# Performance work log

Measured on AMD Instinct MI355X. Metric: run time of the kernel, lower is better.

## Reference

```python
import jax, jax.numpy as jnp
import numpy as np

E, D, H, K = 8, 768, 3072, 2   # num_experts, embed_size, expert_size, top-k
TAU = 1.0
BN, PN = 32, 196

def l2norm(v):
    # F.normalize(p=2, dim=-1), eps=1e-12
    return v / jnp.maximum(jnp.linalg.norm(v, axis=-1, keepdims=True), 1e-12)

def setup_inputs() -> dict:
    key = jax.random.key(0)
    ks = jax.random.split(key, 8)
    s = 0.02  # weight init scale for stability
    return {
        "x": jax.random.normal(ks[0], (BN, PN, D), dtype=jnp.float32),
        "Wlinear": jax.random.normal(ks[1], (D, D), dtype=jnp.float32) * s,
        "learnedE": jax.random.normal(ks[2], (E, D), dtype=jnp.float32),
        "bias": jnp.zeros((BN * PN, E), dtype=jnp.float32),
        "W1": jax.random.normal(ks[3], (E, D, H), dtype=jnp.float32) * s,
        "b1": jnp.zeros((E, H), dtype=jnp.float32),
        "W2": jax.random.normal(ks[4], (E, H, D), dtype=jnp.float32) * s,
        "b2": jnp.zeros((E, D), dtype=jnp.float32),
        "sW1": jax.random.normal(ks[5], (D, H), dtype=jnp.float32) * s,
        "sb1": jnp.zeros((H,), dtype=jnp.float32),
        "sW2": jax.random.normal(ks[6], (H, D), dtype=jnp.float32) * s,
        "sb2": jnp.zeros((D,), dtype=jnp.float32),
    }

def reference(x, Wlinear, learnedE, bias, W1, b1, W2, b2, sW1, sb1, sW2, sb2):
    bn, pn, d = x.shape
    patches = x.reshape(bn * pn, d)                      # [T, D]
    proj = l2norm(patches @ Wlinear.T)                   # router projection
    routed = proj @ l2norm(learnedE).T                   # [T, E] cosine scores
    probs = jax.nn.softmax((routed + bias) / TAU, axis=1)  # eval path (no noise)
    k_probs, k_idx = jax.lax.top_k(probs, K)             # [T, K]
    # combine weights: scatter top-k probs into dense [T, E] gate matrix
    T = probs.shape[0]
    gates = jnp.zeros_like(probs).at[jnp.arange(T)[:, None], k_idx].add(k_probs)
    # expert MLPs computed densely for all experts, masked by gates
    h = jax.nn.gelu(jnp.einsum('td,edh->teh', patches, W1) + b1[None], approximate=False)
    eo = jnp.einsum('teh,ehd->ted', h, W2) + b2[None]    # [T, E, D]
    moe = jnp.einsum('ted,te->td', eo, gates)            # weighted combine
    # shared expert (expert_list[-1]) applied to every token; dropout is identity in eval
    shared = jax.nn.gelu(patches @ sW1 + sb1, approximate=False) @ sW2 + sb2
    return (moe + shared).reshape(bn, pn, d)
```

## Files before the change

kernel.cpp:

```cpp
#include <hip/hip_runtime.h>
#include <hip/hip_bf16.h>

typedef __hip_bfloat16 bf16;
typedef __attribute__((ext_vector_type(8))) short short8;
typedef __attribute__((ext_vector_type(4))) float f32x4;

#define T_TOK 6272
#define D_DIM 768
#define H_DIM 3072
#define NEXP 8
#define MAXTILES 160
#define BKR 64

#define S_BARRIER() __builtin_amdgcn_s_barrier()
#define WAIT_VM0() asm volatile("s_waitcnt vmcnt(0)" ::: "memory")

__device__ __forceinline__ void async16(void* lds, const void* g) {
  __builtin_amdgcn_global_load_lds(
      (const __attribute__((address_space(1))) void*)g,
      (__attribute__((address_space(3))) void*)lds, 16, 0, 0);
}

__device__ __forceinline__ float gelu_f(float x) {
  float z = x * 0.70710678118654752f;
  float az = fabsf(z);
  float t = 1.f / (1.f + 0.3275911f * az);
  float poly = ((((1.061405429f * t - 1.453152027f) * t + 1.421413741f) * t -
                 0.284496736f) * t + 0.254829592f) * t;
  float e = __expf(-az * az);
  float er = 1.f - poly * e;
  er = copysignf(er, z);
  return 0.5f * x * (1.f + er);
}


__global__ void cast_hilo(const float* __restrict__ in, bf16* __restrict__ hi,
                          bf16* __restrict__ lo, int n) {
  int i = blockIdx.x * blockDim.x + threadIdx.x;
  int stride = gridDim.x * blockDim.x;
  for (; i < n; i += stride) {
    float x = in[i];
    bf16 h = __float2bfloat16(x);
    hi[i] = h;
    lo[i] = __float2bfloat16(x - __bfloat162float(h));
  }
}

__global__ void transpose_cast(const float* __restrict__ in, bf16* __restrict__ out,
                               int R, int C) {
  __shared__ float tile[32][33];
  int b = blockIdx.z;
  const float* ib = in + (size_t)b * R * C;
  bf16* ob = out + (size_t)b * R * C;
  int r0 = blockIdx.x * 32, c0 = blockIdx.y * 32;
  int tx = threadIdx.x & 31, ty = threadIdx.x >> 5;
  for (int i = 0; i < 32; i += 8)
    tile[ty + i][tx] = ib[(size_t)(r0 + ty + i) * C + c0 + tx];
  __syncthreads();
  for (int i = 0; i < 32; i += 8)
    ob[(size_t)(c0 + ty + i) * R + r0 + tx] = __float2bfloat16(tile[tx][ty + i]);
}

__global__ void norm_learnedE(const float* __restrict__ lE, float* __restrict__ eHat) {
  int wave = threadIdx.x >> 6, lane = threadIdx.x & 63;
  for (int e = wave; e < NEXP; e += 4) {
    float v[12];
    float ss = 0.f;
    for (int j = 0; j < 12; j++) {
      v[j] = lE[e * D_DIM + lane + 64 * j];
      ss += v[j] * v[j];
    }
    for (int o = 32; o; o >>= 1) ss += __shfl_xor(ss, o);
    float rn = 1.f / fmaxf(sqrtf(ss), 1e-12f);
    for (int j = 0; j < 12; j++) eHat[e * D_DIM + lane + 64 * j] = v[j] * rn;
  }
}


__global__ __launch_bounds__(256, 2) void gemm_router(
    const bf16* __restrict__ pHi, const bf16* __restrict__ pLo,
    const bf16* __restrict__ wHi, const bf16* __restrict__ wLo,
    float* __restrict__ y) {
  __shared__ __align__(16) bf16 As[2][128 * BKR];
  __shared__ __align__(16) bf16 Bs[2][128 * BKR];
  int tid = threadIdx.x, wave = tid >> 6, lane = tid & 63;
  int wr = wave >> 1, wc = wave & 1;
  int rowbase = blockIdx.x * 128, colbase = blockIdx.y * 128;
  int rslot = (lane & 7) ^ (lane >> 3);

  size_t aoff[4], boff[4];
#pragma unroll
  for (int c = 0; c < 4; c++) {
    int row = 32 * wave + 8 * c + (lane >> 3);
    aoff[c] = (size_t)(rowbase + row) * D_DIM + rslot * 8;
    boff[c] = (size_t)(colbase + row) * D_DIM + rslot * 8;
  }

  auto stage = [&](int buf, int ks) {
    int term = ks / 12;
    const bf16* A = (term == 1) ? pLo : pHi;
    const bf16* B = (term == 2) ? wLo : wHi;
    int kk = (ks - term * 12) * BKR;
#pragma unroll
    for (int c = 0; c < 4; c++) {
      async16(&As[buf][(32 * wave + 8 * c) * BKR], A + aoff[c] + kk);
      async16(&Bs[buf][(32 * wave + 8 * c) * BKR], B + boff[c] + kk);
    }
  };

  f32x4 acc[4][4];
#pragma unroll
  for (int m = 0; m < 4; m++)
#pragma unroll
    for (int n = 0; n < 4; n++) acc[m][n] = 0.f;

  stage(0, 0);
  __syncthreads();
  int cur = 0;
  int q = lane >> 4, fr = lane & 15;
  for (int ks = 0; ks < 36; ks++) {
    if (ks < 35) stage(cur ^ 1, ks + 1);
    const bf16* Ac = As[cur];
    const bf16* Bc = Bs[cur];
#pragma unroll
    for (int kh = 0; kh < 2; kh++) {
      short8 af[4], bfr[4];
#pragma unroll
      for (int m = 0; m < 4; m++) {
        int row = wr * 64 + m * 16 + fr;
        int ls = ((kh << 2) + q) ^ (row & 7);
        af[m] = *(const short8*)&Ac[row * BKR + ls * 8];
      }
#pragma unroll
      for (int n = 0; n < 4; n++) {
        int row = wc * 64 + n * 16 + fr;
        int ls = ((kh << 2) + q) ^ (row & 7);
        bfr[n] = *(const short8*)&Bc[row * BKR + ls * 8];
      }
#pragma unroll
      for (int m = 0; m < 4; m++)
#pragma unroll
        for (int n = 0; n < 4; n++)
          acc[m][n] = __builtin_amdgcn_mfma_f32_16x16x32_bf16(af[m], bfr[n], acc[m][n], 0, 0, 0);
    }
    __syncthreads();
    cur ^= 1;
  }
  for (int m = 0; m < 4; m++)
    for (int n = 0; n < 4; n++)
      for (int j = 0; j < 4; j++) {
        int r = rowbase + wr * 64 + m * 16 + (lane >> 4) * 4 + j;
        int c = colbase + wc * 64 + n * 16 + (lane & 15);
        y[(size_t)r * D_DIM + c] = acc[m][n][j];
      }
}


__global__ void router_epi(const float* __restrict__ y, const float* __restrict__ eHat,
                           const float* __restrict__ bias, int* __restrict__ gidx,
                           float* __restrict__ gval, int* __restrict__ counts) {
  int wave = threadIdx.x >> 6, lane = threadIdx.x & 63;
  int t = blockIdx.x * 4 + wave;
  float v[12];
  float ss = 0.f;
  for (int j = 0; j < 12; j++) {
    v[j] = y[(size_t)t * D_DIM + lane + 64 * j];
    ss += v[j] * v[j];
  }
  for (int o = 32; o; o >>= 1) ss += __shfl_xor(ss, o);
  float d[NEXP];
  for (int e = 0; e < NEXP; e++) {
    float s = 0.f;
    for (int j = 0; j < 12; j++) s += v[j] * eHat[e * D_DIM + lane + 64 * j];
    for (int o = 32; o; o >>= 1) s += __shfl_xor(s, o);
    d[e] = s;
  }
  if (lane == 0) {
    float rn = 1.f / fmaxf(sqrtf(ss), 1e-12f);
    float sc[NEXP], mx = -1e30f;
    for (int e = 0; e < NEXP; e++) {
      sc[e] = d[e] * rn + bias[t * NEXP + e];
      mx = fmaxf(mx, sc[e]);
    }
    float p[NEXP], sum = 0.f;
    for (int e = 0; e < NEXP; e++) {
      p[e] = expf(sc[e] - mx);
      sum += p[e];
    }
    float inv = 1.f / sum;
    int i1 = 0;
    for (int e = 1; e < NEXP; e++)
      if (sc[e] > sc[i1]) i1 = e;
    int i2 = -1;
    for (int e = 0; e < NEXP; e++) {
      if (e == i1) continue;
      if (i2 < 0 || sc[e] > sc[i2]) i2 = e;
    }
    gidx[t * 2] = i1;
    gidx[t * 2 + 1] = i2;
    gval[t * 2] = p[i1] * inv;
    gval[t * 2 + 1] = p[i2] * inv;
    atomicAdd(&counts[i1], 1);
    atomicAdd(&counts[i2], 1);
  }
}


__global__ void scan_build(const int* __restrict__ counts, int* __restrict__ segstart,
                           int* __restrict__ cursors, int* __restrict__ tiles,
                           int* __restrict__ numtiles) {
  if (threadIdx.x == 0) {
    int off = 0;
    for (int e = 0; e < NEXP; e++) {
      segstart[e] = off;
      cursors[e] = off;
      off += counts[e];
    }
    segstart[NEXP] = off;
    segstart[NEXP + 1] = off + T_TOK;
    int nt = 0;
    for (int e = 0; e < NEXP + 1; e++) {
      int cnt = (e < NEXP) ? counts[e] : T_TOK;
      int ntl = (cnt + 127) >> 7;
      for (int l = 0; l < ntl; l++) {
        tiles[nt * 2] = e;
        tiles[nt * 2 + 1] = l;
        nt++;
      }
    }
    *numtiles = nt;
  }
}

__global__ void fill_assign(const int* __restrict__ gidx, int* __restrict__ cursors,
                            int* __restrict__ rowtok, int* __restrict__ slot_of) {
  int t = blockIdx.x * 256 + threadIdx.x;
  if (t >= T_TOK) return;
  for (int k = 0; k < 2; k++) {
    int e = gidx[t * 2 + k];
    int pos = atomicAdd(&cursors[e], 1);
    rowtok[pos] = t;
    slot_of[t * 2 + k] = pos;
  }
  rowtok[2 * T_TOK + t] = t;
}



__global__ __launch_bounds__(256, 4) void gemm_ffn1(
    const bf16* __restrict__ pHi, const bf16* __restrict__ W1T,
    const bf16* __restrict__ sW1T, const float* __restrict__ b1,
    const float* __restrict__ sb1, const int* __restrict__ segstart,
    const int* __restrict__ tiles, const int* __restrict__ numtiles,
    const int* __restrict__ rowtok, bf16* __restrict__ hbuf) {
  int gx = blockIdx.x;
  if (gx >= *numtiles) return;
  int seg = tiles[gx * 2], lt = tiles[gx * 2 + 1];
  int s0 = segstart[seg] + lt * 128;
  int send = segstart[seg + 1];
  const bf16* Bw = (seg < NEXP) ? W1T + (size_t)seg * H_DIM * D_DIM : sW1T;
  const float* bb = (seg < NEXP) ? b1 + seg * H_DIM : sb1;

  __shared__ __align__(16) bf16 As[2][128 * 32];
  __shared__ __align__(16) bf16 Bs[2][128 * 32];
  int tid = threadIdx.x, wave = tid >> 6, lane = tid & 63;
  int wr = wave >> 1, wc = wave & 1;
  int colbase = blockIdx.y * 128;
  int q = lane >> 4, fr = lane & 15;
  int g8 = (((lane & 3) ^ ((lane >> 3) & 3))) * 8;
  int ls8 = (q ^ ((fr >> 1) & 3)) * 8;

  const bf16* aptr[2];
  const bf16* bptr[2];
#pragma unroll
  for (int p = 0; p < 2; p++) {
    int r = wave * 32 + p * 16 + (lane >> 2);
    int s = s0 + r;
    if (s > send - 1) s = send - 1;
    aptr[p] = pHi + (size_t)rowtok[s] * D_DIM + g8;
    bptr[p] = Bw + (size_t)(colbase + r) * D_DIM + g8;
  }

  auto stage = [&](int buf, int ks) {
    int kk = ks * 32;
#pragma unroll
    for (int p = 0; p < 2; p++) {
      async16(&As[buf][(wave * 32 + p * 16) * 32], aptr[p] + kk);
      async16(&Bs[buf][(wave * 32 + p * 16) * 32], bptr[p] + kk);
    }
  };

  f32x4 acc[4][4];
#pragma unroll
  for (int m = 0; m < 4; m++)
#pragma unroll
    for (int n = 0; n < 4; n++) acc[m][n] = 0.f;

  stage(0, 0);
  WAIT_VM0();
  S_BARRIER();

#define NT1 24
  for (int ks = 0; ks < NT1; ks++) {
    if (ks + 1 < NT1) stage((ks + 1) & 1, ks + 1);
    const bf16* Ac = As[ks & 1];
    const bf16* Bc = Bs[ks & 1];
    short8 af[4], bfr[4];
#pragma unroll
    for (int m = 0; m < 4; m++)
      af[m] = *(const short8*)&Ac[(wr * 64 + m * 16 + fr) * 32 + ls8];
#pragma unroll
    for (int n = 0; n < 4; n++)
      bfr[n] = *(const short8*)&Bc[(wc * 64 + n * 16 + fr) * 32 + ls8];
    __builtin_amdgcn_s_setprio(1);
#pragma unroll
    for (int m = 0; m < 4; m++)
#pragma unroll
      for (int n = 0; n < 4; n++)
        acc[m][n] = __builtin_amdgcn_mfma_f32_16x16x32_bf16(af[m], bfr[n], acc[m][n], 0, 0, 0);
    __builtin_amdgcn_s_setprio(0);
    WAIT_VM0();
    S_BARRIER();
  }
#pragma unroll
  for (int n = 0; n < 4; n++) {
    int c = colbase + wc * 64 + n * 16 + fr;
    float bv = bb[c];
#pragma unroll
    for (int m = 0; m < 4; m++)
#pragma unroll
      for (int j = 0; j < 4; j++) {
        int s = s0 + wr * 64 + m * 16 + q * 4 + j;
        if (s < send) {
          float xv = acc[m][n][j] + bv;
          hbuf[(size_t)s * H_DIM + c] = __float2bfloat16(gelu_f(xv));
        }
      }
  }
}


__global__ __launch_bounds__(256, 4) void gemm_ffn2(
    const bf16* __restrict__ hbuf, const bf16* __restrict__ W2T,
    const bf16* __restrict__ sW2T, const float* __restrict__ b2,
    const float* __restrict__ sb2, const int* __restrict__ segstart,
    const int* __restrict__ tiles, const int* __restrict__ numtiles,
    float* __restrict__ moebuf) {
  int gx = blockIdx.x;
  if (gx >= *numtiles) return;
  int seg = tiles[gx * 2], lt = tiles[gx * 2 + 1];
  int s0 = segstart[seg] + lt * 128;
  int send = segstart[seg + 1];
  const bf16* Bw = (seg < NEXP) ? W2T + (size_t)seg * H_DIM * D_DIM : sW2T;
  const float* bb = (seg < NEXP) ? b2 + seg * D_DIM : sb2;

  __shared__ __align__(16) bf16 As[2][128 * 32];
  __shared__ __align__(16) bf16 Bs[2][128 * 32];
  int tid = threadIdx.x, wave = tid >> 6, lane = tid & 63;
  int wr = wave >> 1, wc = wave & 1;
  int colbase = blockIdx.y * 128;
  int q = lane >> 4, fr = lane & 15;
  int g8 = (((lane & 3) ^ ((lane >> 3) & 3))) * 8;
  int ls8 = (q ^ ((fr >> 1) & 3)) * 8;

  const bf16* aptr[2];
  const bf16* bptr[2];
#pragma unroll
  for (int p = 0; p < 2; p++) {
    int r = wave * 32 + p * 16 + (lane >> 2);
    int s = s0 + r;
    if (s > send - 1) s = send - 1;
    aptr[p] = hbuf + (size_t)s * H_DIM + g8;
    bptr[p] = Bw + (size_t)(colbase + r) * H_DIM + g8;
  }

  auto stage = [&](int buf, int ks) {
    int kk = ks * 32;
#pragma unroll
    for (int p = 0; p < 2; p++) {
      async16(&As[buf][(wave * 32 + p * 16) * 32], aptr[p] + kk);
      async16(&Bs[buf][(wave * 32 + p * 16) * 32], bptr[p] + kk);
    }
  };

  f32x4 acc[4][4];
#pragma unroll
  for (int m = 0; m < 4; m++)
#pragma unroll
    for (int n = 0; n < 4; n++) acc[m][n] = 0.f;

  stage(0, 0);
  WAIT_VM0();
  S_BARRIER();

#define NT2 96
  for (int ks = 0; ks < NT2; ks++) {
    if (ks + 1 < NT2) stage((ks + 1) & 1, ks + 1);
    const bf16* Ac = As[ks & 1];
    const bf16* Bc = Bs[ks & 1];
    short8 af[4], bfr[4];
#pragma unroll
    for (int m = 0; m < 4; m++)
      af[m] = *(const short8*)&Ac[(wr * 64 + m * 16 + fr) * 32 + ls8];
#pragma unroll
    for (int n = 0; n < 4; n++)
      bfr[n] = *(const short8*)&Bc[(wc * 64 + n * 16 + fr) * 32 + ls8];
    __builtin_amdgcn_s_setprio(1);
#pragma unroll
    for (int m = 0; m < 4; m++)
#pragma unroll
      for (int n = 0; n < 4; n++)
        acc[m][n] = __builtin_amdgcn_mfma_f32_16x16x32_bf16(af[m], bfr[n], acc[m][n], 0, 0, 0);
    __builtin_amdgcn_s_setprio(0);
    WAIT_VM0();
    S_BARRIER();
  }
#pragma unroll
  for (int n = 0; n < 4; n++) {
    int c = colbase + wc * 64 + n * 16 + fr;
    float bv = bb[c];
#pragma unroll
    for (int m = 0; m < 4; m++)
#pragma unroll
      for (int j = 0; j < 4; j++) {
        int s = s0 + wr * 64 + m * 16 + q * 4 + j;
        if (s < send) moebuf[(size_t)s * D_DIM + c] = acc[m][n][j] + bv;
      }
  }
}


__global__ void combine_out(const float* __restrict__ moebuf, const float* __restrict__ gval,
                            const int* __restrict__ slot_of, float* __restrict__ out) {
  int i = blockIdx.x * 256 + threadIdx.x;
  const int total = T_TOK * (D_DIM / 4);
  if (i >= total) return;
  int t = i / (D_DIM / 4), c = i % (D_DIM / 4);
  float g0 = gval[2 * t], g1 = gval[2 * t + 1];
  int sA = slot_of[2 * t], sB = slot_of[2 * t + 1];
  const f32x4* pa = (const f32x4*)(moebuf + (size_t)sA * D_DIM) + c;
  const f32x4* pb = (const f32x4*)(moebuf + (size_t)sB * D_DIM) + c;
  const f32x4* ps = (const f32x4*)(moebuf + (size_t)(2 * T_TOK + t) * D_DIM) + c;
  f32x4 r = g0 * (*pa) + g1 * (*pb) + *ps;
  ((f32x4*)out)[i] = r;
}


extern "C" void kernel_launch(void* const* d_in, const int* in_sizes, int n_in,
                              void* d_out, int out_size, void* d_ws, size_t ws_size,
                              hipStream_t stream) {
  const float* x = (const float*)d_in[0];
  const float* Wlinear = (const float*)d_in[1];
  const float* learnedE = (const float*)d_in[2];
  const float* bias = (const float*)d_in[3];
  const float* W1 = (const float*)d_in[4];
  const float* b1 = (const float*)d_in[5];
  const float* W2 = (const float*)d_in[6];
  const float* b2 = (const float*)d_in[7];
  const float* sW1 = (const float*)d_in[8];
  const float* sb1 = (const float*)d_in[9];
  const float* sW2 = (const float*)d_in[10];
  const float* sb2 = (const float*)d_in[11];
  float* out = (float*)d_out;

  char* ws = (char*)d_ws;
  size_t off = 0;
  auto alloc = [&](size_t bytes) {
    char* p = ws + off;
    off += (bytes + 255) & ~(size_t)255;
    return p;
  };
  float* eHat = (float*)alloc(8 * 768 * 4);
  bf16* pHi = (bf16*)alloc((size_t)T_TOK * D_DIM * 2);
  bf16* pLo = (bf16*)alloc((size_t)T_TOK * D_DIM * 2);
  bf16* wHi = (bf16*)alloc((size_t)D_DIM * D_DIM * 2);
  bf16* wLo = (bf16*)alloc((size_t)D_DIM * D_DIM * 2);
  bf16* W1T = (bf16*)alloc((size_t)NEXP * D_DIM * H_DIM * 2);
  bf16* W2T = (bf16*)alloc((size_t)NEXP * D_DIM * H_DIM * 2);
  bf16* sW1T = (bf16*)alloc((size_t)D_DIM * H_DIM * 2);
  bf16* sW2T = (bf16*)alloc((size_t)D_DIM * H_DIM * 2);
  float* y = (float*)alloc((size_t)T_TOK * D_DIM * 4);
  bf16* hbuf = (bf16*)alloc((size_t)3 * T_TOK * H_DIM * 2);
  float* moebuf = (float*)alloc((size_t)3 * T_TOK * D_DIM * 4);
  int* gidx = (int*)alloc(T_TOK * 2 * 4);
  float* gval = (float*)alloc(T_TOK * 2 * 4);
  int* rowtok = (int*)alloc(3 * T_TOK * 4);
  int* slot_of = (int*)alloc(T_TOK * 2 * 4);
  int* counts = (int*)alloc(8 * 4);
  int* segstart = (int*)alloc(10 * 4);
  int* cursors = (int*)alloc(8 * 4);
  int* numtiles = (int*)alloc(4);
  int* tiles = (int*)alloc(MAXTILES * 2 * 4);
  (void)ws_size; (void)in_sizes; (void)n_in; (void)out_size;

  hipMemsetAsync(counts, 0, 8 * 4, stream);
  norm_learnedE<<<1, 256, 0, stream>>>(learnedE, eHat);
  cast_hilo<<<2048, 256, 0, stream>>>(x, pHi, pLo, T_TOK * D_DIM);
  cast_hilo<<<1024, 256, 0, stream>>>(Wlinear, wHi, wLo, D_DIM * D_DIM);
  transpose_cast<<<dim3(D_DIM / 32, H_DIM / 32, NEXP), 256, 0, stream>>>(W1, W1T, D_DIM, H_DIM);
  transpose_cast<<<dim3(H_DIM / 32, D_DIM / 32, NEXP), 256, 0, stream>>>(W2, W2T, H_DIM, D_DIM);
  transpose_cast<<<dim3(D_DIM / 32, H_DIM / 32, 1), 256, 0, stream>>>(sW1, sW1T, D_DIM, H_DIM);
  transpose_cast<<<dim3(H_DIM / 32, D_DIM / 32, 1), 256, 0, stream>>>(sW2, sW2T, H_DIM, D_DIM);

  gemm_router<<<dim3(T_TOK / 128, D_DIM / 128), 256, 0, stream>>>(pHi, pLo, wHi, wLo, y);
  router_epi<<<T_TOK / 4, 256, 0, stream>>>(y, eHat, bias, gidx, gval, counts);
  scan_build<<<1, 64, 0, stream>>>(counts, segstart, cursors, tiles, numtiles);
  fill_assign<<<(T_TOK + 255) / 256, 256, 0, stream>>>(gidx, cursors, rowtok, slot_of);

  gemm_ffn1<<<dim3(MAXTILES, H_DIM / 128), 256, 0, stream>>>(
      pHi, W1T, sW1T, b1, sb1, segstart, tiles, numtiles, rowtok, hbuf);
  gemm_ffn2<<<dim3(MAXTILES, D_DIM / 128), 256, 0, stream>>>(
      hbuf, W2T, sW2T, b2, sb2, segstart, tiles, numtiles, moebuf);

  combine_out<<<(T_TOK * (D_DIM / 4) + 255) / 256, 256, 0, stream>>>(moebuf, gval, slot_of, out);
}
```

Before: 719.1 us.

## Enlarge grouped FFN GEMM tiles to 256x256 with deeper async LDS pipeline

Both expert FFN GEMMs move from 128x128 tiles with 256 threads to 256x256 tiles with 512 threads. Each tile row is now 256 tokens, so the tile list and launch grid shrink to match. The double-buffered K loop becomes a 4-buffer pipeline: A and B loads are issued as separate half-stages and waited on with partial vmcnt counts, and each wave's 8x4 accumulator block is computed in two halves. The goal is more operand reuse per global load and more latency hiding. In exchange it uses about 128KB of LDS per block and more accumulator registers, and launches far fewer blocks (the FFN2 grid in particular may not fill the GPU).

```diff
diff --git a/kernel.cpp b/kernel.cpp
--- a/kernel.cpp
+++ b/kernel.cpp
@@ -9,10 +9,12 @@
 #define D_DIM 768
 #define H_DIM 3072
 #define NEXP 8
-#define MAXTILES 160
+#define MAXT 96
 #define BKR 64
 
 #define S_BARRIER() __builtin_amdgcn_s_barrier()
+#define WAIT_VM6() asm volatile("s_waitcnt vmcnt(6)" ::: "memory")
+#define WAIT_VM4() asm volatile("s_waitcnt vmcnt(4)" ::: "memory")
 #define WAIT_VM0() asm volatile("s_waitcnt vmcnt(0)" ::: "memory")
 
 __device__ __forceinline__ void async16(void* lds, const void* g) {
@@ -221,7 +223,7 @@
     int nt = 0;
     for (int e = 0; e < NEXP + 1; e++) {
       int cnt = (e < NEXP) ? counts[e] : T_TOK;
-      int ntl = (cnt + 127) >> 7;
+      int ntl = (cnt + 255) >> 8;
       for (int l = 0; l < ntl; l++) {
         tiles[nt * 2] = e;
         tiles[nt * 2 + 1] = l;
@@ -247,7 +249,7 @@
 
 
 
-__global__ __launch_bounds__(256, 4) void gemm_ffn1(
+__global__ __launch_bounds__(512, 2) void gemm_ffn1(
     const bf16* __restrict__ pHi, const bf16* __restrict__ W1T,
     const bf16* __restrict__ sW1T, const float* __restrict__ b1,
     const float* __restrict__ sb1, const int* __restrict__ segstart,
@@ -256,62 +258,67 @@
   int gx = blockIdx.x;
   if (gx >= *numtiles) return;
   int seg = tiles[gx * 2], lt = tiles[gx * 2 + 1];
-  int s0 = segstart[seg] + lt * 128;
+  int s0 = segstart[seg] + lt * 256;
   int send = segstart[seg + 1];
   const bf16* Bw = (seg < NEXP) ? W1T + (size_t)seg * H_DIM * D_DIM : sW1T;
   const float* bb = (seg < NEXP) ? b1 + seg * H_DIM : sb1;
 
-  __shared__ __align__(16) bf16 As[2][128 * 32];
-  __shared__ __align__(16) bf16 Bs[2][128 * 32];
+  __shared__ __align__(16) bf16 As[4][256 * 32];
+  __shared__ __align__(16) bf16 Bs[4][256 * 32];
   int tid = threadIdx.x, wave = tid >> 6, lane = tid & 63;
-  int wr = wave >> 1, wc = wave & 1;
-  int colbase = blockIdx.y * 128;
+  int wr = wave >> 2, wc = wave & 3;
+  int colbase = blockIdx.y * 256;
   int q = lane >> 4, fr = lane & 15;
-  int g8 = (((lane & 3) ^ ((lane >> 3) & 3))) * 8;
+  int g8 = ((tid & 3) ^ ((tid >> 3) & 3)) * 8;
+  int row0 = tid >> 2;
+  int slot8 = (tid & 3) * 8;
   int ls8 = (q ^ ((fr >> 1) & 3)) * 8;
 
-  const bf16* aptr[2];
-  const bf16* bptr[2];
-#pragma unroll
-  for (int p = 0; p < 2; p++) {
-    int r = wave * 32 + p * 16 + (lane >> 2);
-    int s = s0 + r;
-    if (s > send - 1) s = send - 1;
-    aptr[p] = pHi + (size_t)rowtok[s] * D_DIM + g8;
-    bptr[p] = Bw + (size_t)(colbase + r) * D_DIM + g8;
-  }
-
-  auto stage = [&](int buf, int ks) {
-    int kk = ks * 32;
-#pragma unroll
-    for (int p = 0; p < 2; p++) {
-      async16(&As[buf][(wave * 32 + p * 16) * 32], aptr[p] + kk);
-      async16(&Bs[buf][(wave * 32 + p * 16) * 32], bptr[p] + kk);
+  int sA0 = s0 + row0; if (sA0 > send - 1) sA0 = send - 1;
+  int sA1 = s0 + row0 + 128; if (sA1 > send - 1) sA1 = send - 1;
+  const bf16* aptr0 = pHi + (size_t)rowtok[sA0] * D_DIM + g8;
+  const bf16* aptr1 = pHi + (size_t)rowtok[sA1] * D_DIM + g8;
+  const bf16* bptr0 = Bw + (size_t)(colbase + row0) * D_DIM + g8;
+  const bf16* bptr1 = Bw + (size_t)(colbase + row0 + 128) * D_DIM + g8;
+
+  auto stage = [&](int s) {
+    int ts = s >> 1;
+    int kk = ts * 32;
+    int buf = ts & 3;
+    if ((s & 1) == 0) {
+      async16(&As[buf][row0 * 32 + slot8], aptr0 + kk);
+      async16(&As[buf][(row0 + 128) * 32 + slot8], aptr1 + kk);
+    } else {
+      async16(&Bs[buf][row0 * 32 + slot8], bptr0 + kk);
+      async16(&Bs[buf][(row0 + 128) * 32 + slot8], bptr1 + kk);
     }
   };
 
-  f32x4 acc[4][4];
-#pragma unroll
-  for (int m = 0; m < 4; m++)
+  f32x4 acc[8][4];
+#pragma unroll
+  for (int m = 0; m < 8; m++)
 #pragma unroll
     for (int n = 0; n < 4; n++) acc[m][n] = 0.f;
 
-  stage(0, 0);
   WAIT_VM0();
-  S_BARRIER();
+  stage(0); stage(1); stage(2); stage(3); stage(4);
 
 #define NT1 24
-  for (int ks = 0; ks < NT1; ks++) {
-    if (ks + 1 < NT1) stage((ks + 1) & 1, ks + 1);
-    const bf16* Ac = As[ks & 1];
-    const bf16* Bc = Bs[ks & 1];
-    short8 af[4], bfr[4];
-#pragma unroll
-    for (int m = 0; m < 4; m++)
-      af[m] = *(const short8*)&Ac[(wr * 64 + m * 16 + fr) * 32 + ls8];
+  for (int t = 0; t < NT1; t++) {
+    if (t + 2 < NT1) { WAIT_VM6(); }
+    else if (t + 1 < NT1) { WAIT_VM4(); }
+    else { WAIT_VM0(); }
+    S_BARRIER();
+    const bf16* Ac = As[t & 3];
+    const bf16* Bc = Bs[t & 3];
+    short8 bfr[4], af[4];
 #pragma unroll
     for (int n = 0; n < 4; n++)
       bfr[n] = *(const short8*)&Bc[(wc * 64 + n * 16 + fr) * 32 + ls8];
+#pragma unroll
+    for (int m = 0; m < 4; m++)
+      af[m] = *(const short8*)&Ac[(wr * 128 + m * 16 + fr) * 32 + ls8];
+    if (2 * t + 5 < 2 * NT1) stage(2 * t + 5);
     __builtin_amdgcn_s_setprio(1);
 #pragma unroll
     for (int m = 0; m < 4; m++)
@@ -319,7 +326,19 @@
       for (int n = 0; n < 4; n++)
         acc[m][n] = __builtin_amdgcn_mfma_f32_16x16x32_bf16(af[m], bfr[n], acc[m][n], 0, 0, 0);
     __builtin_amdgcn_s_setprio(0);
-    WAIT_VM0();
+    S_BARRIER();
+#pragma unroll
+    for (int m = 0; m < 4; m++)
+      af[m] = *(const short8*)&Ac[(wr * 128 + (m + 4) * 16 + fr) * 32 + ls8];
+    if (2 * t + 6 < 2 * NT1) stage(2 * t + 6);
+    S_BARRIER();
+    __builtin_amdgcn_s_setprio(1);
+#pragma unroll
+    for (int m = 0; m < 4; m++)
+#pragma unroll
+      for (int n = 0; n < 4; n++)
+        acc[m + 4][n] = __builtin_amdgcn_mfma_f32_16x16x32_bf16(af[m], bfr[n], acc[m + 4][n], 0, 0, 0);
+    __builtin_amdgcn_s_setprio(0);
     S_BARRIER();
   }
 #pragma unroll
@@ -327,10 +346,10 @@
     int c = colbase + wc * 64 + n * 16 + fr;
     float bv = bb[c];
 #pragma unroll
-    for (int m = 0; m < 4; m++)
+    for (int m = 0; m < 8; m++)
 #pragma unroll
       for (int j = 0; j < 4; j++) {
-        int s = s0 + wr * 64 + m * 16 + q * 4 + j;
+        int s = s0 + wr * 128 + m * 16 + q * 4 + j;
         if (s < send) {
           float xv = acc[m][n][j] + bv;
           hbuf[(size_t)s * H_DIM + c] = __float2bfloat16(gelu_f(xv));
@@ -340,7 +359,7 @@
 }
 
 
-__global__ __launch_bounds__(256, 4) void gemm_ffn2(
+__global__ __launch_bounds__(512, 2) void gemm_ffn2(
     const bf16* __restrict__ hbuf, const bf16* __restrict__ W2T,
     const bf16* __restrict__ sW2T, const float* __restrict__ b2,
     const float* __restrict__ sb2, const int* __restrict__ segstart,
@@ -349,62 +368,67 @@
   int gx = blockIdx.x;
   if (gx >= *numtiles) return;
   int seg = tiles[gx * 2], lt = tiles[gx * 2 + 1];
-  int s0 = segstart[seg] + lt * 128;
+  int s0 = segstart[seg] + lt * 256;
   int send = segstart[seg + 1];
   const bf16* Bw = (seg < NEXP) ? W2T + (size_t)seg * H_DIM * D_DIM : sW2T;
   const float* bb = (seg < NEXP) ? b2 + seg * D_DIM : sb2;
 
-  __shared__ __align__(16) bf16 As[2][128 * 32];
-  __shared__ __align__(16) bf16 Bs[2][128 * 32];
+  __shared__ __align__(16) bf16 As[4][256 * 32];
+  __shared__ __align__(16) bf16 Bs[4][256 * 32];
   int tid = threadIdx.x, wave = tid >> 6, lane = tid & 63;
-  int wr = wave >> 1, wc = wave & 1;
-  int colbase = blockIdx.y * 128;
+  int wr = wave >> 2, wc = wave & 3;
+  int colbase = blockIdx.y * 256;
   int q = lane >> 4, fr = lane & 15;
-  int g8 = (((lane & 3) ^ ((lane >> 3) & 3))) * 8;
+  int g8 = ((tid & 3) ^ ((tid >> 3) & 3)) * 8;
+  int row0 = tid >> 2;
+  int slot8 = (tid & 3) * 8;
   int ls8 = (q ^ ((fr >> 1) & 3)) * 8;
 
-  const bf16* aptr[2];
-  const bf16* bptr[2];
-#pragma unroll
-  for (int p = 0; p < 2; p++) {
-    int r = wave * 32 + p * 16 + (lane >> 2);
-    int s = s0 + r;
-    if (s > send - 1) s = send - 1;
-    aptr[p] = hbuf + (size_t)s * H_DIM + g8;
-    bptr[p] = Bw + (size_t)(colbase + r) * H_DIM + g8;
-  }
-
-  auto stage = [&](int buf, int ks) {
-    int kk = ks * 32;
-#pragma unroll
-    for (int p = 0; p < 2; p++) {
-      async16(&As[buf][(wave * 32 + p * 16) * 32], aptr[p] + kk);
-      async16(&Bs[buf][(wave * 32 + p * 16) * 32], bptr[p] + kk);
+  int sA0 = s0 + row0; if (sA0 > send - 1) sA0 = send - 1;
+  int sA1 = s0 + row0 + 128; if (sA1 > send - 1) sA1 = send - 1;
+  const bf16* aptr0 = hbuf + (size_t)sA0 * H_DIM + g8;
+  const bf16* aptr1 = hbuf + (size_t)sA1 * H_DIM + g8;
+  const bf16* bptr0 = Bw + (size_t)(colbase + row0) * H_DIM + g8;
+  const bf16* bptr1 = Bw + (size_t)(colbase + row0 + 128) * H_DIM + g8;
+
+  auto stage = [&](int s) {
+    int ts = s >> 1;
+    int kk = ts * 32;
+    int buf = ts & 3;
+    if ((s & 1) == 0) {
+      async16(&As[buf][row0 * 32 + slot8], aptr0 + kk);
+      async16(&As[buf][(row0 + 128) * 32 + slot8], aptr1 + kk);
+    } else {
+      async16(&Bs[buf][row0 * 32 + slot8], bptr0 + kk);
+      async16(&Bs[buf][(row0 + 128) * 32 + slot8], bptr1 + kk);
     }
   };
 
-  f32x4 acc[4][4];
-#pragma unroll
-  for (int m = 0; m < 4; m++)
+  f32x4 acc[8][4];
+#pragma unroll
+  for (int m = 0; m < 8; m++)
 #pragma unroll
     for (int n = 0; n < 4; n++) acc[m][n] = 0.f;
 
-  stage(0, 0);
   WAIT_VM0();
-  S_BARRIER();
+  stage(0); stage(1); stage(2); stage(3); stage(4);
 
 #define NT2 96
-  for (int ks = 0; ks < NT2; ks++) {
-    if (ks + 1 < NT2) stage((ks + 1) & 1, ks + 1);
-    const bf16* Ac = As[ks & 1];
-    const bf16* Bc = Bs[ks & 1];
-    short8 af[4], bfr[4];
-#pragma unroll
-    for (int m = 0; m < 4; m++)
-      af[m] = *(const short8*)&Ac[(wr * 64 + m * 16 + fr) * 32 + ls8];
+  for (int t = 0; t < NT2; t++) {
+    if (t + 2 < NT2) { WAIT_VM6(); }
+    else if (t + 1 < NT2) { WAIT_VM4(); }
+    else { WAIT_VM0(); }
+    S_BARRIER();
+    const bf16* Ac = As[t & 3];
+    const bf16* Bc = Bs[t & 3];
+    short8 bfr[4], af[4];
 #pragma unroll
     for (int n = 0; n < 4; n++)
       bfr[n] = *(const short8*)&Bc[(wc * 64 + n * 16 + fr) * 32 + ls8];
+#pragma unroll
+    for (int m = 0; m < 4; m++)
+      af[m] = *(const short8*)&Ac[(wr * 128 + m * 16 + fr) * 32 + ls8];
+    if (2 * t + 5 < 2 * NT2) stage(2 * t + 5);
     __builtin_amdgcn_s_setprio(1);
 #pragma unroll
     for (int m = 0; m < 4; m++)
@@ -412,7 +436,19 @@
       for (int n = 0; n < 4; n++)
         acc[m][n] = __builtin_amdgcn_mfma_f32_16x16x32_bf16(af[m], bfr[n], acc[m][n], 0, 0, 0);
     __builtin_amdgcn_s_setprio(0);
-    WAIT_VM0();
+    S_BARRIER();
+#pragma unroll
+    for (int m = 0; m < 4; m++)
+      af[m] = *(const short8*)&Ac[(wr * 128 + (m + 4) * 16 + fr) * 32 + ls8];
+    if (2 * t + 6 < 2 * NT2) stage(2 * t + 6);
+    S_BARRIER();
+    __builtin_amdgcn_s_setprio(1);
+#pragma unroll
+    for (int m = 0; m < 4; m++)
+#pragma unroll
+      for (int n = 0; n < 4; n++)
+        acc[m + 4][n] = __builtin_amdgcn_mfma_f32_16x16x32_bf16(af[m], bfr[n], acc[m + 4][n], 0, 0, 0);
+    __builtin_amdgcn_s_setprio(0);
     S_BARRIER();
   }
 #pragma unroll
@@ -420,10 +456,10 @@
     int c = colbase + wc * 64 + n * 16 + fr;
     float bv = bb[c];
 #pragma unroll
-    for (int m = 0; m < 4; m++)
+    for (int m = 0; m < 8; m++)
 #pragma unroll
       for (int j = 0; j < 4; j++) {
-        int s = s0 + wr * 64 + m * 16 + q * 4 + j;
+        int s = s0 + wr * 128 + m * 16 + q * 4 + j;
         if (s < send) moebuf[(size_t)s * D_DIM + c] = acc[m][n][j] + bv;
       }
   }
@@ -490,7 +526,7 @@
   int* segstart = (int*)alloc(10 * 4);
   int* cursors = (int*)alloc(8 * 4);
   int* numtiles = (int*)alloc(4);
-  int* tiles = (int*)alloc(MAXTILES * 2 * 4);
+  int* tiles = (int*)alloc(MAXT * 2 * 4);
   (void)ws_size; (void)in_sizes; (void)n_in; (void)out_size;
 
   hipMemsetAsync(counts, 0, 8 * 4, stream);
@@ -507,9 +543,9 @@
   scan_build<<<1, 64, 0, stream>>>(counts, segstart, cursors, tiles, numtiles);
   fill_assign<<<(T_TOK + 255) / 256, 256, 0, stream>>>(gidx, cursors, rowtok, slot_of);
 
-  gemm_ffn1<<<dim3(MAXTILES, H_DIM / 128), 256, 0, stream>>>(
+  gemm_ffn1<<<dim3(MAXT, H_DIM / 256), 512, 0, stream>>>(
       pHi, W1T, sW1T, b1, sb1, segstart, tiles, numtiles, rowtok, hbuf);
-  gemm_ffn2<<<dim3(MAXTILES, D_DIM / 128), 256, 0, stream>>>(
+  gemm_ffn2<<<dim3(MAXT, D_DIM / 256), 512, 0, stream>>>(
       hbuf, W2T, sW2T, b2, sb2, segstart, tiles, numtiles, moebuf);
 
   combine_out<<<(T_TOK * (D_DIM / 4) + 255) / 256, 256, 0, stream>>>(moebuf, gval, slot_of, out);
```

Measured after the change: 804.7 us. +11.9%, slower.

## Remap GEMM block indices for XCD-aware grouped tile scheduling

Applied to the files above, without the earlier changes.

Adds an XCD-aware remapping of linear block IDs so consecutive work items land on the same XCD. Within each XCD, tiles are swizzled into groups of row tiles sharing column tiles. This applies to the router GEMM and both expert FFN GEMMs, which now launch with flattened or reshaped grids. The aim is better L2 reuse of A and B tiles on MI355X's multi-XCD layout, at the cost of some index arithmetic and a dependence on the round-robin block-to-XCD dispatch assumption.

```diff
diff --git a/kernel.cpp b/kernel.cpp
--- a/kernel.cpp
+++ b/kernel.cpp
@@ -31,6 +31,13 @@
   float er = 1.f - poly * e;
   er = copysignf(er, z);
   return 0.5f * x * (1.f + er);
+}
+
+__device__ __forceinline__ int xcd_work(int orig, int nwr) {
+  if (orig >= nwr) return -1;
+  int xcd = orig & 7, pos = orig >> 3;
+  int q = nwr >> 3, r = nwr & 7;
+  return (xcd < r ? xcd * (q + 1) : r * (q + 1) + (xcd - r) * q) + pos;
 }
 
 
@@ -81,11 +88,19 @@
     const bf16* __restrict__ pHi, const bf16* __restrict__ pLo,
     const bf16* __restrict__ wHi, const bf16* __restrict__ wLo,
     float* __restrict__ y) {
+  int work = xcd_work(blockIdx.x, 294);
+  int tileG = work / 48;
+  int rem = work - tileG * 48;
+  int base = tileG * 8;
+  int gl = 49 - base; if (gl > 8) gl = 8;
+  int colb = rem / gl;
+  int rowt = base + rem % gl;
+
   __shared__ __align__(16) bf16 As[2][128 * BKR];
   __shared__ __align__(16) bf16 Bs[2][128 * BKR];
   int tid = threadIdx.x, wave = tid >> 6, lane = tid & 63;
   int wr = wave >> 1, wc = wave & 1;
-  int rowbase = blockIdx.x * 128, colbase = blockIdx.y * 128;
+  int rowbase = rowt * 128, colbase = colb * 128;
   int rslot = (lane & 7) ^ (lane >> 3);
 
   size_t aoff[4], boff[4];
@@ -253,8 +268,17 @@
     const float* __restrict__ sb1, const int* __restrict__ segstart,
     const int* __restrict__ tiles, const int* __restrict__ numtiles,
     const int* __restrict__ rowtok, bf16* __restrict__ hbuf) {
-  int gx = blockIdx.x;
-  if (gx >= *numtiles) return;
+  const int NC = 24, G = 16;
+  int nt = *numtiles;
+  int work = xcd_work(blockIdx.x + NC * blockIdx.y, nt * NC);
+  if (work < 0) return;
+  int tileG = work / (NC * G);
+  int rem = work - tileG * (NC * G);
+  int tbase = tileG * G;
+  int gl = nt - tbase; if (gl > G) gl = G;
+  int colb = rem / gl;
+  int gx = tbase + rem % gl;
+
   int seg = tiles[gx * 2], lt = tiles[gx * 2 + 1];
   int s0 = segstart[seg] + lt * 128;
   int send = segstart[seg + 1];
@@ -265,7 +289,7 @@
   __shared__ __align__(16) bf16 Bs[2][128 * 32];
   int tid = threadIdx.x, wave = tid >> 6, lane = tid & 63;
   int wr = wave >> 1, wc = wave & 1;
-  int colbase = blockIdx.y * 128;
+  int colbase = colb * 128;
   int q = lane >> 4, fr = lane & 15;
   int g8 = (((lane & 3) ^ ((lane >> 3) & 3))) * 8;
   int ls8 = (q ^ ((fr >> 1) & 3)) * 8;
@@ -346,8 +370,17 @@
     const float* __restrict__ sb2, const int* __restrict__ segstart,
     const int* __restrict__ tiles, const int* __restrict__ numtiles,
     float* __restrict__ moebuf) {
-  int gx = blockIdx.x;
-  if (gx >= *numtiles) return;
+  const int NC = 6, G = 4;
+  int nt = *numtiles;
+  int work = xcd_work(blockIdx.x + NC * blockIdx.y, nt * NC);
+  if (work < 0) return;
+  int tileG = work / (NC * G);
+  int rem = work - tileG * (NC * G);
+  int tbase = tileG * G;
+  int gl = nt - tbase; if (gl > G) gl = G;
+  int colb = rem / gl;
+  int gx = tbase + rem % gl;
+
   int seg = tiles[gx * 2], lt = tiles[gx * 2 + 1];
   int s0 = segstart[seg] + lt * 128;
   int send = segstart[seg + 1];
@@ -358,7 +391,7 @@
   __shared__ __align__(16) bf16 Bs[2][128 * 32];
   int tid = threadIdx.x, wave = tid >> 6, lane = tid & 63;
   int wr = wave >> 1, wc = wave & 1;
-  int colbase = blockIdx.y * 128;
+  int colbase = colb * 128;
   int q = lane >> 4, fr = lane & 15;
   int g8 = (((lane & 3) ^ ((lane >> 3) & 3))) * 8;
   int ls8 = (q ^ ((fr >> 1) & 3)) * 8;
@@ -502,14 +535,14 @@
   transpose_cast<<<dim3(D_DIM / 32, H_DIM / 32, 1), 256, 0, stream>>>(sW1, sW1T, D_DIM, H_DIM);
   transpose_cast<<<dim3(H_DIM / 32, D_DIM / 32, 1), 256, 0, stream>>>(sW2, sW2T, H_DIM, D_DIM);
 
-  gemm_router<<<dim3(T_TOK / 128, D_DIM / 128), 256, 0, stream>>>(pHi, pLo, wHi, wLo, y);
+  gemm_router<<<294, 256, 0, stream>>>(pHi, pLo, wHi, wLo, y);
   router_epi<<<T_TOK / 4, 256, 0, stream>>>(y, eHat, bias, gidx, gval, counts);
   scan_build<<<1, 64, 0, stream>>>(counts, segstart, cursors, tiles, numtiles);
   fill_assign<<<(T_TOK + 255) / 256, 256, 0, stream>>>(gidx, cursors, rowtok, slot_of);
 
-  gemm_ffn1<<<dim3(MAXTILES, H_DIM / 128), 256, 0, stream>>>(
+  gemm_ffn1<<<dim3(24, MAXTILES), 256, 0, stream>>>(
       pHi, W1T, sW1T, b1, sb1, segstart, tiles, numtiles, rowtok, hbuf);
-  gemm_ffn2<<<dim3(MAXTILES, D_DIM / 128), 256, 0, stream>>>(
+  gemm_ffn2<<<dim3(6, MAXTILES), 256, 0, stream>>>(
       hbuf, W2T, sW2T, b2, sb2, segstart, tiles, numtiles, moebuf);
 
   combine_out<<<(T_TOK * (D_DIM / 4) + 255) / 256, 256, 0, stream>>>(moebuf, gval, slot_of, out);
```

After: 671.7 us, median of 2. 6.6% less time.
